# Kernel tuning notes

Hardware: AMD Instinct MI355X
Metric: run time of the kernel (lower is better)

Reference implementation:

```python
import jax, jax.numpy as jnp
import numpy as np

D_MODEL = 768
N_HEADS = 12
HEAD_DIM = D_MODEL // N_HEADS


def setup_inputs() -> dict:
    key = jax.random.key(0)
    ks = jax.random.split(key, 9)
    s = 1.0 / np.sqrt(D_MODEL)
    inp = {
        "inputs": jax.random.normal(ks[0], (1, 4096, D_MODEL), dtype=jnp.float32),
        "Wq": jax.random.uniform(ks[1], (D_MODEL, D_MODEL), jnp.float32, -s, s),
        "bq": jax.random.uniform(ks[2], (D_MODEL,), jnp.float32, -s, s),
        "Wk": jax.random.uniform(ks[3], (D_MODEL, D_MODEL), jnp.float32, -s, s),
        "bk": jax.random.uniform(ks[4], (D_MODEL,), jnp.float32, -s, s),
        "Wv": jax.random.uniform(ks[5], (D_MODEL, D_MODEL), jnp.float32, -s, s),
        "bv": jax.random.uniform(ks[6], (D_MODEL,), jnp.float32, -s, s),
        "Wo": jax.random.uniform(ks[7], (D_MODEL, D_MODEL), jnp.float32, -s, s),
        "bo": jax.random.uniform(ks[8], (D_MODEL,), jnp.float32, -s, s),
    }
    return inp


def reference(inputs, Wq, bq, Wk, bk, Wv, bv, Wo, bo):
    B, S, D = inputs.shape
    H, Hd = N_HEADS, HEAD_DIM

    def split_heads(x):  # [B,S,D] -> [B,H,S,Hd]
        return x.reshape(B, S, H, Hd).transpose(0, 2, 1, 3)

    # nn.Linear computes x @ W.T + b
    Q = split_heads(inputs @ Wq.T + bq)
    K = split_heads(inputs @ Wk.T + bk)
    V = split_heads(inputs @ Wv.T + bv)

    scores = jnp.einsum("bhsd,bhtd->bhst", Q, K) / jnp.sqrt(jnp.float32(Hd))
    causal = jnp.tril(jnp.ones((S, S), dtype=bool))  # True = keep
    scores = jnp.where(causal, scores, -jnp.inf)
    attn = jax.nn.softmax(scores, axis=-1)  # dropout is identity in eval

    out = jnp.einsum("bhst,bhtd->bhsd", attn, V)
    out = out.transpose(0, 2, 1, 3).reshape(B, S, D)
    return out @ Wo.T + bo
```

## Files before the change

### kernel.cpp

```cpp
#include <hip/hip_runtime.h>
#include <stdint.h>

#define SEQ 4096
#define DM 768
#define NH 12
#define HD 64

typedef unsigned short u16;
typedef short short8 __attribute__((ext_vector_type(8)));
typedef float floatx4 __attribute__((ext_vector_type(4)));
typedef float floatx16 __attribute__((ext_vector_type(16)));

__device__ inline u16 f2b(float f) {
  union { float f; uint32_t u; } v; v.f = f;
  uint32_t u = v.u;
  return (u16)((u + 0x7fffu + ((u >> 16) & 1u)) >> 16);
}

__device__ inline float b2f(u16 x) {
  union { uint32_t u; float f; } v; v.u = ((uint32_t)x) << 16;
  return v.f;
}

#if defined(__has_builtin)
#if __has_builtin(__builtin_amdgcn_cvt_pk_bf16_f32)
#define HAVE_PK_BF16 1
#endif
#endif

__device__ inline uint32_t pk_bf16(float a, float b) {
#ifdef HAVE_PK_BF16
  typedef __bf16 bf16x2_t __attribute__((ext_vector_type(2)));
  union { bf16x2_t v; uint32_t u; } c;
  c.v = __builtin_amdgcn_cvt_pk_bf16_f32(a, b);
  return c.u;
#else
  uint32_t r;
  asm("v_cvt_pk_bf16_f32 %0, %1, %2" : "=v"(r) : "v"(a), "v"(b));
  return r;
#endif
}

__device__ inline void pl32swap(uint32_t& a, uint32_t& b) {
  asm("v_permlane32_swap_b32 %0, %1" : "+v"(a), "+v"(b));
}

__device__ inline void load_lds16(const void* g, void* l) {
  __builtin_amdgcn_global_load_lds(
      (const __attribute__((address_space(1))) uint32_t*)g,
      (__attribute__((address_space(3))) uint32_t*)l, 16, 0, 0);
}

__global__ __launch_bounds__(256) void convert_all(
    const float* __restrict__ X, const float* __restrict__ Wq,
    const float* __restrict__ Wk, const float* __restrict__ Wv,
    const float* __restrict__ Wo,
    u16* __restrict__ Xb, u16* __restrict__ Wqb, u16* __restrict__ Wkb,
    u16* __restrict__ Wvb, u16* __restrict__ Wob) {
  int t = blockIdx.x * 256 + threadIdx.x;
  const int NX = SEQ * DM / 4;
  const int NW = DM * DM / 4;
  const float* src; u16* dst; int off;
  if (t < NX)               { src = X;  dst = Xb;  off = t; }
  else if (t < NX + NW)     { src = Wq; dst = Wqb; off = t - NX; }
  else if (t < NX + 2 * NW) { src = Wk; dst = Wkb; off = t - NX - NW; }
  else if (t < NX + 3 * NW) { src = Wv; dst = Wvb; off = t - NX - 2 * NW; }
  else if (t < NX + 4 * NW) { src = Wo; dst = Wob; off = t - NX - 3 * NW; }
  else return;
  float4 v = *(const float4*)(src + (size_t)off * 4);
  uint2 o;
  o.x = pk_bf16(v.x, v.y);
  o.y = pk_bf16(v.z, v.w);
  *(uint2*)(dst + (size_t)off * 4) = o;
}

__global__ __launch_bounds__(256) void gemm_qkv(
    const u16* __restrict__ Xb,
    const u16* __restrict__ Wqb, const u16* __restrict__ Wkb,
    const u16* __restrict__ Wvb,
    const float* __restrict__ bq, const float* __restrict__ bk,
    const float* __restrict__ bv,
    u16* __restrict__ Qh, u16* __restrict__ Kh, u16* __restrict__ VtG) {
  const int p = blockIdx.x;
  const int wg = (p & 7) * 72 + (p >> 3);
  const int mb = wg / 18, nz = wg % 18;
  const int z = nz / 6;
  const int n0 = (nz % 6) * 128;
  const int m0 = mb * 128;

  const u16* W; const float* bias;
  if (z == 0)      { W = Wqb; bias = bq; }
  else if (z == 1) { W = Wkb; bias = bk; }
  else             { W = Wvb; bias = bv; }

  __shared__ u16 smem[32768];
  u16* As = smem;
  u16* Bs = smem + 16384;

  const int tid = threadIdx.x;
  const int wave = tid >> 6, lane = tid & 63;
  const int g = lane >> 4, ln = lane & 15;
  const int wm = (wave & 1) * 64, wn = (wave >> 1) * 64;
  const int srow = lane >> 3;
  const int schunk = (lane & 7) ^ srow;
  const int swz = ln & 7;

  floatx4 acc[4][4] = {};

  auto stage = [&](int k0, int buf) {
#pragma unroll
    for (int i = 0; i < 4; ++i) {
      int u = wave * 4 + i;
      load_lds16(Xb + (size_t)(m0 + u * 8 + srow) * DM + k0 + schunk * 8,
                 As + buf * 8192 + u * 512);
      load_lds16(W + (size_t)(n0 + u * 8 + srow) * DM + k0 + schunk * 8,
                 Bs + buf * 8192 + u * 512);
    }
  };

  stage(0, 0);

  for (int kt = 0; kt < 12; ++kt) {
    const int cur = kt & 1;
    __syncthreads();
    if (kt < 11) stage((kt + 1) * 64, cur ^ 1);
    const u16* Ac = As + cur * 8192;
    const u16* Bc = Bs + cur * 8192;
#pragma unroll
    for (int kh = 0; kh < 2; ++kh) {
      short8 af[4], bf[4];
#pragma unroll
      for (int mi = 0; mi < 4; ++mi)
        af[mi] = *(const short8*)(Ac + (wm + mi * 16 + ln) * 64 +
                                  ((kh * 4 + g) ^ swz) * 8);
#pragma unroll
      for (int ni = 0; ni < 4; ++ni)
        bf[ni] = *(const short8*)(Bc + (wn + ni * 16 + ln) * 64 +
                                  ((kh * 4 + g) ^ swz) * 8);
#pragma unroll
      for (int mi = 0; mi < 4; ++mi)
#pragma unroll
        for (int ni = 0; ni < 4; ++ni)
          acc[mi][ni] = __builtin_amdgcn_mfma_f32_16x16x32_bf16(
              af[mi], bf[ni], acc[mi][ni], 0, 0, 0);
    }
  }

  const float qscale = 0.125f * 1.44269504089f;
  const int hh0 = n0 >> 6;
  __syncthreads();
  u16* ep = smem;

  if (z == 2) {
#pragma unroll
    for (int mi = 0; mi < 4; ++mi) {
      int row0 = wm + mi * 16 + g * 4;
#pragma unroll
      for (int ni = 0; ni < 4; ++ni) {
        int col = wn + ni * 16 + ln;
        float b = bias[n0 + col];
        uint2 o;
        o.x = pk_bf16(acc[mi][ni][0] + b, acc[mi][ni][1] + b);
        o.y = pk_bf16(acc[mi][ni][2] + b, acc[mi][ni][3] + b);
        *(uint2*)(ep + col * 136 + row0) = o;
      }
    }
    __syncthreads();
#pragma unroll
    for (int t = 0; t < 8; ++t) {
      int unit = tid + t * 256;
      int dcol = unit >> 4, ch = unit & 15;
      int head = hh0 + (dcol >> 6), d = dcol & 63;
      short8 v = *(const short8*)(ep + dcol * 136 + ch * 8);
      *(short8*)(VtG + ((size_t)(head * 64 + d)) * SEQ + m0 + ch * 8) = v;
    }
  } else {
    u16* out = (z == 0) ? Qh : Kh;
    float cs = (z == 0) ? qscale : 1.0f;
#pragma unroll
    for (int mi = 0; mi < 4; ++mi) {
      int row0 = wm + mi * 16 + g * 4;
#pragma unroll
      for (int ni = 0; ni < 4; ++ni) {
        int col = wn + ni * 16 + ln;
        float b = bias[n0 + col];
        uint32_t w0 = pk_bf16((acc[mi][ni][0] + b) * cs, (acc[mi][ni][1] + b) * cs);
        uint32_t w1 = pk_bf16((acc[mi][ni][2] + b) * cs, (acc[mi][ni][3] + b) * cs);
        ep[(row0 + 0) * 136 + col] = (u16)w0;
        ep[(row0 + 1) * 136 + col] = (u16)(w0 >> 16);
        ep[(row0 + 2) * 136 + col] = (u16)w1;
        ep[(row0 + 3) * 136 + col] = (u16)(w1 >> 16);
      }
    }
    __syncthreads();
#pragma unroll
    for (int t = 0; t < 8; ++t) {
      int unit = tid + t * 256;
      int row = unit >> 4, ch = unit & 15;
      int head = hh0 + (ch >> 3), d0 = (ch & 7) * 8;
      short8 v = *(const short8*)(ep + row * 136 + ch * 8);
      *(short8*)(out + ((size_t)head * SEQ + m0 + row) * HD + d0) = v;
    }
  }
}

#define CHUNK 16
#define M0 40.0f
__global__ __launch_bounds__(256, 4) void attn_chunk(
    const u16* __restrict__ Qh, const u16* __restrict__ Kh,
    const u16* __restrict__ VtG, u16* __restrict__ Opart,
    float* __restrict__ Lp) {
  const int p = blockIdx.y * NH + blockIdx.x;
  const int slot = p % 24, cyc = p / 24;
  const int qq = 3 * (slot & 7) + (slot >> 3);
  const int h = qq >> 1;
  const int b = 79 - (cyc * 2 + (qq & 1));
  int qB, ci;
  if (b < 8)       { qB = b;               ci = 0; }
  else if (b < 24) { int r = b - 8;  qB = 8 + (r >> 1); ci = r & 1; }
  else if (b < 48) { int r = b - 24; int d = r / 3; qB = 16 + d; ci = r - d * 3; }
  else             { int r = b - 48; qB = 24 + (r >> 2); ci = r & 3; }
  const int kb0 = ci * CHUNK;
  const int kb1 = min(kb0 + CHUNK, 2 * qB + 2);
  const int slot2 = (h * 32 + qB) * 4 + ci;

  const int tid = threadIdx.x, wave = tid >> 6, lane = tid & 63;
  const int hi = lane >> 5, lq = lane & 31;
  const int q0 = qB * 128;
  const int qwave = q0 + wave * 32;
  const int srow = lane >> 3;
  const int schunk = (lane & 7) ^ srow;
  const int rsw = lane & 7;

  __shared__ u16 Ks[2 * 4096];
  __shared__ u16 Vt[2 * 4096];

  const int qglob = qwave + lq;
  const u16* Qbase = Qh + ((size_t)h * SEQ + qglob) * HD;
  short8 aq[4];
#pragma unroll
  for (int s = 0; s < 4; ++s)
    aq[s] = *(const short8*)(Qbase + s * 16 + hi * 8);

  floatx16 oacc[2] = {};
  floatx4 lacc = {};

  const size_t kbase = (size_t)h * SEQ * HD;
  const size_t vbase = (size_t)h * 64 * SEQ;

  auto stage = [&](int kbIdx, int buf) {
#pragma unroll
    for (int i = 0; i < 2; ++i) {
      int u = wave * 2 + i;
      load_lds16(Kh + kbase + (size_t)(kbIdx * 64 + u * 8 + srow) * HD + schunk * 8,
                 Ks + buf * 4096 + u * 512);
      load_lds16(VtG + vbase + (size_t)(u * 8 + srow) * SEQ + kbIdx * 64 + schunk * 8,
                 Vt + buf * 4096 + u * 512);
    }
  };

  stage(kb0, 0);

  for (int kb = kb0; kb < kb1; ++kb) {
    const int cur = (kb - kb0) & 1;
    __syncthreads();
    if (kb + 1 < kb1) stage(kb + 1, cur ^ 1);

    const u16* Kc = Ks + cur * 4096;
    const u16* Vc = Vt + cur * 4096;

    if (kb * 64 > qwave + 31) continue;

    floatx16 st[2];
#pragma unroll
    for (int kblk = 0; kblk < 2; ++kblk)
#pragma unroll
      for (int r2 = 0; r2 < 16; ++r2) st[kblk][r2] = -M0;
    __builtin_amdgcn_s_setprio(1);
#pragma unroll
    for (int s = 0; s < 4; ++s)
#pragma unroll
      for (int kblk = 0; kblk < 2; ++kblk) {
        short8 kf = *(const short8*)(Kc + (kblk * 32 + lq) * 64 +
                                     ((s * 2 + hi) ^ rsw) * 8);
        st[kblk] = __builtin_amdgcn_mfma_f32_32x32x16_bf16(kf, aq[s], st[kblk],
                                                           0, 0, 0);
      }
    __builtin_amdgcn_s_setprio(0);

    if (kb * 64 + 63 > qwave) {
#pragma unroll
      for (int kblk = 0; kblk < 2; ++kblk)
#pragma unroll
        for (int r2 = 0; r2 < 16; ++r2) {
          int key = kb * 64 + kblk * 32 + (r2 & 3) + 8 * (r2 >> 2) + 4 * hi;
          if (key > qglob) st[kblk][r2] = -1e30f;
        }
    }

    uint32_t w[2][8];
#pragma unroll
    for (int kblk = 0; kblk < 2; ++kblk) {
#pragma unroll
      for (int r2 = 0; r2 < 16; ++r2)
        st[kblk][r2] = __builtin_amdgcn_exp2f(st[kblk][r2]);
#pragma unroll
      for (int r2 = 0; r2 < 4; ++r2)
        lacc[r2] += st[kblk][r2] + st[kblk][4 + r2] + st[kblk][8 + r2] +
                    st[kblk][12 + r2];
#pragma unroll
      for (int i = 0; i < 8; ++i)
        w[kblk][i] = pk_bf16(st[kblk][2 * i], st[kblk][2 * i + 1]);
    }

    __builtin_amdgcn_s_setprio(1);
#pragma unroll
    for (int ks = 0; ks < 4; ++ks) {
      const int kblk = ks >> 1, base = (ks & 1) * 4;
      uint32_t d0 = w[kblk][base + 0], d2 = w[kblk][base + 2];
      uint32_t d1 = w[kblk][base + 1], d3 = w[kblk][base + 3];
      pl32swap(d0, d2);
      pl32swap(d1, d3);
      union { uint32_t u[4]; short8 s; } bp;
      bp.u[0] = d0; bp.u[1] = d1; bp.u[2] = d2; bp.u[3] = d3;
#pragma unroll
      for (int dblk = 0; dblk < 2; ++dblk) {
        short8 vf = *(const short8*)(Vc + (dblk * 32 + lq) * 64 +
                                     ((ks * 2 + hi) ^ rsw) * 8);
        oacc[dblk] = __builtin_amdgcn_mfma_f32_32x32x16_bf16(vf, bp.s, oacc[dblk],
                                                             0, 0, 0);
      }
    }
    __builtin_amdgcn_s_setprio(0);
  }

  float l_i = lacc[0] + lacc[1] + lacc[2] + lacc[3];
  l_i += __shfl_xor(l_i, 32);

  float inv = 1.f / l_i;
  int qloc = wave * 32 + lq;
  u16* Op = Opart + (size_t)slot2 * 8192 + qloc * 64;
#pragma unroll
  for (int dblk = 0; dblk < 2; ++dblk)
#pragma unroll
    for (int qd = 0; qd < 4; ++qd) {
      uint2 o;
      o.x = pk_bf16(oacc[dblk][qd * 4 + 0] * inv, oacc[dblk][qd * 4 + 1] * inv);
      o.y = pk_bf16(oacc[dblk][qd * 4 + 2] * inv, oacc[dblk][qd * 4 + 3] * inv);
      *(uint2*)(Op + dblk * 32 + qd * 8 + hi * 4) = o;
    }
  if (hi == 0) Lp[(size_t)slot2 * 128 + qloc] = l_i;
}

__global__ __launch_bounds__(256) void attn_merge(
    const u16* __restrict__ Opart, const float* __restrict__ Lp,
    u16* __restrict__ Ob) {
  const int h = blockIdx.x, qB = blockIdx.y;
  const int n = (qB >> 3) + 1;
  const int base = (h * 32 + qB) * 4;
  const int q = threadIdx.x >> 1;
  const int d0 = (threadIdx.x & 1) * 32;

  float L = 0.f;
  for (int i = 0; i < n; ++i) L += Lp[(size_t)(base + i) * 128 + q];
  float invL = 1.f / L;

  float acc[32];
#pragma unroll
  for (int jj = 0; jj < 32; ++jj) acc[jj] = 0.f;
  for (int i = 0; i < n; ++i) {
    float wi = Lp[(size_t)(base + i) * 128 + q] * invL;
    const u16* src = Opart + (size_t)(base + i) * 8192 + q * 64 + d0;
#pragma unroll
    for (int c = 0; c < 4; ++c) {
      short8 a = ((const short8*)src)[c];
#pragma unroll
      for (int jj = 0; jj < 8; ++jj) acc[c * 8 + jj] += wi * b2f((u16)a[jj]);
    }
  }

  u16* dst = Ob + (size_t)(qB * 128 + q) * DM + h * HD + d0;
#pragma unroll
  for (int c = 0; c < 4; ++c) {
    uint4 o;
    o.x = pk_bf16(acc[c * 8 + 0], acc[c * 8 + 1]);
    o.y = pk_bf16(acc[c * 8 + 2], acc[c * 8 + 3]);
    o.z = pk_bf16(acc[c * 8 + 4], acc[c * 8 + 5]);
    o.w = pk_bf16(acc[c * 8 + 6], acc[c * 8 + 7]);
    ((uint4*)dst)[c] = o;
  }
}

__global__ __launch_bounds__(256) void gemm_out(
    const u16* __restrict__ Ab, const u16* __restrict__ Wob,
    const float* __restrict__ bo, float* __restrict__ Cout) {
  __shared__ u16 smem[16384];

  const int tid = threadIdx.x;
  const int wave = tid >> 6, lane = tid & 63;
  const int g = lane >> 4, ln = lane & 15;
  const int m0 = blockIdx.y * 64, n0 = blockIdx.x * 64;
  const int wm = (wave & 1) * 32, wn = (wave >> 1) * 32;
  const int srow = lane >> 3;
  const int schunk = (lane & 7) ^ srow;
  const int swz = ln & 7;

  floatx4 acc[2][2] = {};

#pragma unroll
  for (int i = 0; i < 2; ++i) {
    int u = wave * 2 + i;
    load_lds16(Ab + (size_t)(m0 + u * 8 + srow) * DM + schunk * 8, smem + u * 512);
    load_lds16(Wob + (size_t)(n0 + u * 8 + srow) * DM + schunk * 8,
               smem + 8192 + u * 512);
  }

  for (int kt = 0; kt < 12; ++kt) {
    const int cur = kt & 1;
    __syncthreads();
    if (kt < 11) {
      const int k0 = (kt + 1) * 64, nb = cur ^ 1;
#pragma unroll
      for (int i = 0; i < 2; ++i) {
        int u = wave * 2 + i;
        load_lds16(Ab + (size_t)(m0 + u * 8 + srow) * DM + k0 + schunk * 8,
                   smem + nb * 4096 + u * 512);
        load_lds16(Wob + (size_t)(n0 + u * 8 + srow) * DM + k0 + schunk * 8,
                   smem + 8192 + nb * 4096 + u * 512);
      }
    }
    const u16* Ac = smem + cur * 4096;
    const u16* Bc = smem + 8192 + cur * 4096;
    short8 af[2][2], bf[2][2];
#pragma unroll
    for (int mi = 0; mi < 2; ++mi)
#pragma unroll
      for (int kh = 0; kh < 2; ++kh)
        af[mi][kh] = *(const short8*)(Ac + (wm + mi * 16 + ln) * 64 +
                                      ((kh * 4 + g) ^ swz) * 8);
#pragma unroll
    for (int ni = 0; ni < 2; ++ni)
#pragma unroll
      for (int kh = 0; kh < 2; ++kh)
        bf[ni][kh] = *(const short8*)(Bc + (wn + ni * 16 + ln) * 64 +
                                      ((kh * 4 + g) ^ swz) * 8);
#pragma unroll
    for (int kh = 0; kh < 2; ++kh)
#pragma unroll
      for (int mi = 0; mi < 2; ++mi)
#pragma unroll
        for (int ni = 0; ni < 2; ++ni)
          acc[mi][ni] = __builtin_amdgcn_mfma_f32_16x16x32_bf16(
              af[mi][kh], bf[ni][kh], acc[mi][ni], 0, 0, 0);
  }

#pragma unroll
  for (int mi = 0; mi < 2; ++mi) {
    int row = m0 + wm + mi * 16 + g * 4;
#pragma unroll
    for (int ni = 0; ni < 2; ++ni) {
      int col = n0 + wn + ni * 16 + ln;
      float b = bo[col];
#pragma unroll
      for (int r = 0; r < 4; ++r)
        Cout[(size_t)(row + r) * DM + col] = acc[mi][ni][r] + b;
    }
  }
}

extern "C" void kernel_launch(void* const* d_in, const int* in_sizes, int n_in,
                              void* d_out, int out_size, void* d_ws, size_t ws_size,
                              hipStream_t stream) {
  const float* X  = (const float*)d_in[0];
  const float* Wq = (const float*)d_in[1];
  const float* bq = (const float*)d_in[2];
  const float* Wk = (const float*)d_in[3];
  const float* bk = (const float*)d_in[4];
  const float* Wv = (const float*)d_in[5];
  const float* bv = (const float*)d_in[6];
  const float* Wo = (const float*)d_in[7];
  const float* bo = (const float*)d_in[8];
  float* out = (float*)d_out;

  char* ws = (char*)d_ws;
  u16* Wob = (u16*)ws; ws += (size_t)DM * DM * 2;
  u16* Qh  = (u16*)ws; ws += (size_t)NH * SEQ * HD * 2;
  u16* Kh  = (u16*)ws; ws += (size_t)NH * SEQ * HD * 2;
  u16* VtG = (u16*)ws; ws += (size_t)NH * SEQ * HD * 2;
  u16* Ob  = (u16*)ws; ws += (size_t)SEQ * DM * 2;
  float* Lp = (float*)ws; ws += (size_t)NH * 32 * 4 * 128 * 4;
  char* ovl = ws;
  u16* Xb  = (u16*)ovl;
  u16* Wqb = Xb + (size_t)SEQ * DM;
  u16* Wkb = Wqb + (size_t)DM * DM;
  u16* Wvb = Wkb + (size_t)DM * DM;
  u16* Opart = (u16*)ovl;

  convert_all<<<5376, 256, 0, stream>>>(X, Wq, Wk, Wv, Wo, Xb, Wqb, Wkb, Wvb, Wob);

  gemm_qkv<<<576, 256, 0, stream>>>(Xb, Wqb, Wkb, Wvb, bq, bk, bv, Qh, Kh, VtG);

  dim3 ga(NH, 80);
  attn_chunk<<<ga, 256, 0, stream>>>(Qh, Kh, VtG, Opart, Lp);

  dim3 gm(NH, 32);
  attn_merge<<<gm, 256, 0, stream>>>(Opart, Lp, Ob);

  dim3 go(DM / 64, SEQ / 64);
  gemm_out<<<go, 256, 0, stream>>>(Ob, Wob, bo, out);
}
```

Measured before the change: 166.2 us.

## Fuse split-K attention merge into chunk kernel via last-arriver atomic counter

Removes the separate attn_merge launch. Each attention chunk block increments a per-(head, query-block) counter, and the last block to arrive combines the partial outputs with the L weights and writes Ob directly. Query blocks with a single chunk skip the partial buffers and write Ob straight away. The counters are zeroed inside convert_all. This saves a kernel launch and the partial round trip for small query blocks, at the cost of threadfences, an atomic, and a serial merge tail in the last-arriving block.

Result: slower. 236.0 us (+42.0%).

```diff
diff --git a/kernel.cpp b/kernel.cpp
--- a/kernel.cpp
+++ b/kernel.cpp
@@ -56,7 +56,10 @@
     const float* __restrict__ Wk, const float* __restrict__ Wv,
     const float* __restrict__ Wo,
     u16* __restrict__ Xb, u16* __restrict__ Wqb, u16* __restrict__ Wkb,
-    u16* __restrict__ Wvb, u16* __restrict__ Wob) {
+    u16* __restrict__ Wvb, u16* __restrict__ Wob, uint32_t* __restrict__ Cnt) {
+  if (blockIdx.x == 0) {
+    for (int i = threadIdx.x; i < NH * 32; i += 256) Cnt[i] = 0;
+  }
   int t = blockIdx.x * 256 + threadIdx.x;
   const int NX = SEQ * DM / 4;
   const int NW = DM * DM / 4;
@@ -209,7 +212,8 @@
 __global__ __launch_bounds__(256, 4) void attn_chunk(
     const u16* __restrict__ Qh, const u16* __restrict__ Kh,
     const u16* __restrict__ VtG, u16* __restrict__ Opart,
-    float* __restrict__ Lp) {
+    float* __restrict__ Lp, uint32_t* __restrict__ Cnt,
+    u16* __restrict__ Ob) {
   const int p = blockIdx.y * NH + blockIdx.x;
   const int slot = p % 24, cyc = p / 24;
   const int qq = 3 * (slot & 7) + (slot >> 3);
@@ -222,6 +226,7 @@
   else             { int r = b - 48; qB = 24 + (r >> 2); ci = r & 3; }
   const int kb0 = ci * CHUNK;
   const int kb1 = min(kb0 + CHUNK, 2 * qB + 2);
+  const int n_part = (qB >> 3) + 1;
   const int slot2 = (h * 32 + qB) * 4 + ci;
 
   const int tid = threadIdx.x, wave = tid >> 6, lane = tid & 63;
@@ -234,6 +239,7 @@
 
   __shared__ u16 Ks[2 * 4096];
   __shared__ u16 Vt[2 * 4096];
+  __shared__ int who;
 
   const int qglob = qwave + lq;
   const u16* Qbase = Qh + ((size_t)h * SEQ + qglob) * HD;
@@ -339,6 +345,21 @@
 
   float inv = 1.f / l_i;
   int qloc = wave * 32 + lq;
+
+  if (n_part == 1) {
+    u16* dst = Ob + (size_t)(q0 + qloc) * DM + h * HD;
+#pragma unroll
+    for (int dblk = 0; dblk < 2; ++dblk)
+#pragma unroll
+      for (int qd = 0; qd < 4; ++qd) {
+        uint2 o;
+        o.x = pk_bf16(oacc[dblk][qd * 4 + 0] * inv, oacc[dblk][qd * 4 + 1] * inv);
+        o.y = pk_bf16(oacc[dblk][qd * 4 + 2] * inv, oacc[dblk][qd * 4 + 3] * inv);
+        *(uint2*)(dst + dblk * 32 + qd * 8 + hi * 4) = o;
+      }
+    return;
+  }
+
   u16* Op = Opart + (size_t)slot2 * 8192 + qloc * 64;
 #pragma unroll
   for (int dblk = 0; dblk < 2; ++dblk)
@@ -350,44 +371,50 @@
       *(uint2*)(Op + dblk * 32 + qd * 8 + hi * 4) = o;
     }
   if (hi == 0) Lp[(size_t)slot2 * 128 + qloc] = l_i;
-}
-
-__global__ __launch_bounds__(256) void attn_merge(
-    const u16* __restrict__ Opart, const float* __restrict__ Lp,
-    u16* __restrict__ Ob) {
-  const int h = blockIdx.x, qB = blockIdx.y;
-  const int n = (qB >> 3) + 1;
-  const int base = (h * 32 + qB) * 4;
-  const int q = threadIdx.x >> 1;
-  const int d0 = (threadIdx.x & 1) * 32;
-
-  float L = 0.f;
-  for (int i = 0; i < n; ++i) L += Lp[(size_t)(base + i) * 128 + q];
-  float invL = 1.f / L;
-
-  float acc[32];
-#pragma unroll
-  for (int jj = 0; jj < 32; ++jj) acc[jj] = 0.f;
-  for (int i = 0; i < n; ++i) {
-    float wi = Lp[(size_t)(base + i) * 128 + q] * invL;
-    const u16* src = Opart + (size_t)(base + i) * 8192 + q * 64 + d0;
+
+  __syncthreads();
+  if (tid == 0) {
+    __threadfence();
+    uint32_t old = atomicAdd(&Cnt[h * 32 + qB], 1u);
+    who = (old == (uint32_t)(n_part - 1)) ? 1 : 0;
+  }
+  __syncthreads();
+  if (!who) return;
+  __threadfence();
+
+  {
+    const int base = (h * 32 + qB) * 4;
+    const int q = tid >> 1;
+    const int d0 = (tid & 1) * 32;
+
+    float L = 0.f;
+    for (int i = 0; i < n_part; ++i) L += Lp[(size_t)(base + i) * 128 + q];
+    float invL = 1.f / L;
+
+    float acc2[32];
+#pragma unroll
+    for (int jj = 0; jj < 32; ++jj) acc2[jj] = 0.f;
+    for (int i = 0; i < n_part; ++i) {
+      float wi = Lp[(size_t)(base + i) * 128 + q] * invL;
+      const u16* src = Opart + (size_t)(base + i) * 8192 + q * 64 + d0;
+#pragma unroll
+      for (int c = 0; c < 4; ++c) {
+        short8 a = ((const short8*)src)[c];
+#pragma unroll
+        for (int jj = 0; jj < 8; ++jj) acc2[c * 8 + jj] += wi * b2f((u16)a[jj]);
+      }
+    }
+
+    u16* dst = Ob + (size_t)(q0 + q) * DM + h * HD + d0;
 #pragma unroll
     for (int c = 0; c < 4; ++c) {
-      short8 a = ((const short8*)src)[c];
-#pragma unroll
-      for (int jj = 0; jj < 8; ++jj) acc[c * 8 + jj] += wi * b2f((u16)a[jj]);
-    }
-  }
-
-  u16* dst = Ob + (size_t)(qB * 128 + q) * DM + h * HD + d0;
-#pragma unroll
-  for (int c = 0; c < 4; ++c) {
-    uint4 o;
-    o.x = pk_bf16(acc[c * 8 + 0], acc[c * 8 + 1]);
-    o.y = pk_bf16(acc[c * 8 + 2], acc[c * 8 + 3]);
-    o.z = pk_bf16(acc[c * 8 + 4], acc[c * 8 + 5]);
-    o.w = pk_bf16(acc[c * 8 + 6], acc[c * 8 + 7]);
-    ((uint4*)dst)[c] = o;
+      uint4 o;
+      o.x = pk_bf16(acc2[c * 8 + 0], acc2[c * 8 + 1]);
+      o.y = pk_bf16(acc2[c * 8 + 2], acc2[c * 8 + 3]);
+      o.z = pk_bf16(acc2[c * 8 + 4], acc2[c * 8 + 5]);
+      o.w = pk_bf16(acc2[c * 8 + 6], acc2[c * 8 + 7]);
+      ((uint4*)dst)[c] = o;
+    }
   }
 }
 
@@ -489,6 +516,7 @@
   u16* VtG = (u16*)ws; ws += (size_t)NH * SEQ * HD * 2;
   u16* Ob  = (u16*)ws; ws += (size_t)SEQ * DM * 2;
   float* Lp = (float*)ws; ws += (size_t)NH * 32 * 4 * 128 * 4;
+  uint32_t* Cnt = (uint32_t*)ws; ws += (size_t)NH * 32 * 4;
   char* ovl = ws;
   u16* Xb  = (u16*)ovl;
   u16* Wqb = Xb + (size_t)SEQ * DM;
@@ -496,15 +524,13 @@
   u16* Wvb = Wkb + (size_t)DM * DM;
   u16* Opart = (u16*)ovl;
 
-  convert_all<<<5376, 256, 0, stream>>>(X, Wq, Wk, Wv, Wo, Xb, Wqb, Wkb, Wvb, Wob);
+  convert_all<<<5376, 256, 0, stream>>>(X, Wq, Wk, Wv, Wo, Xb, Wqb, Wkb, Wvb,
+                                        Wob, Cnt);
 
   gemm_qkv<<<576, 256, 0, stream>>>(Xb, Wqb, Wkb, Wvb, bq, bk, bv, Qh, Kh, VtG);
 
   dim3 ga(NH, 80);
-  attn_chunk<<<ga, 256, 0, stream>>>(Qh, Kh, VtG, Opart, Lp);
-
-  dim3 gm(NH, 32);
-  attn_merge<<<gm, 256, 0, stream>>>(Opart, Lp, Ob);
+  attn_chunk<<<ga, 256, 0, stream>>>(Qh, Kh, VtG, Opart, Lp, Cnt, Ob);
 
   dim3 go(DM / 64, SEQ / 64);
   gemm_out<<<go, 256, 0, stream>>>(Ob, Wob, bo, out);
```

## Fuse split-KV attention merge into output projection GEMM A-tile loading

Applied to the files above, without the earlier changes.

Removes the separate attn_merge kernel and the Ob intermediate buffer. The attention kernel now writes unnormalized partial outputs. The output GEMM sums up to four partials per row as it loads each A tile, scales them by the inverse total denominator and writes the bf16 result into LDS, overlapped with the MFMA work on the other buffer. This saves a kernel launch and a global write/read round trip of the merged activations. In exchange, every column block of the GEMM redoes the merge, so partial reads are multiplied, and the A loads become register-staged instead of direct-to-LDS.

New measurement: 191.7 us. 1.15x slower.

```diff
diff --git a/kernel.cpp b/kernel.cpp
--- a/kernel.cpp
+++ b/kernel.cpp
@@ -337,7 +337,6 @@
   float l_i = lacc[0] + lacc[1] + lacc[2] + lacc[3];
   l_i += __shfl_xor(l_i, 32);
 
-  float inv = 1.f / l_i;
   int qloc = wave * 32 + lq;
   u16* Op = Opart + (size_t)slot2 * 8192 + qloc * 64;
 #pragma unroll
@@ -345,54 +344,16 @@
 #pragma unroll
     for (int qd = 0; qd < 4; ++qd) {
       uint2 o;
-      o.x = pk_bf16(oacc[dblk][qd * 4 + 0] * inv, oacc[dblk][qd * 4 + 1] * inv);
-      o.y = pk_bf16(oacc[dblk][qd * 4 + 2] * inv, oacc[dblk][qd * 4 + 3] * inv);
+      o.x = pk_bf16(oacc[dblk][qd * 4 + 0], oacc[dblk][qd * 4 + 1]);
+      o.y = pk_bf16(oacc[dblk][qd * 4 + 2], oacc[dblk][qd * 4 + 3]);
       *(uint2*)(Op + dblk * 32 + qd * 8 + hi * 4) = o;
     }
   if (hi == 0) Lp[(size_t)slot2 * 128 + qloc] = l_i;
 }
 
-__global__ __launch_bounds__(256) void attn_merge(
+__global__ __launch_bounds__(256) void gemm_out(
     const u16* __restrict__ Opart, const float* __restrict__ Lp,
-    u16* __restrict__ Ob) {
-  const int h = blockIdx.x, qB = blockIdx.y;
-  const int n = (qB >> 3) + 1;
-  const int base = (h * 32 + qB) * 4;
-  const int q = threadIdx.x >> 1;
-  const int d0 = (threadIdx.x & 1) * 32;
-
-  float L = 0.f;
-  for (int i = 0; i < n; ++i) L += Lp[(size_t)(base + i) * 128 + q];
-  float invL = 1.f / L;
-
-  float acc[32];
-#pragma unroll
-  for (int jj = 0; jj < 32; ++jj) acc[jj] = 0.f;
-  for (int i = 0; i < n; ++i) {
-    float wi = Lp[(size_t)(base + i) * 128 + q] * invL;
-    const u16* src = Opart + (size_t)(base + i) * 8192 + q * 64 + d0;
-#pragma unroll
-    for (int c = 0; c < 4; ++c) {
-      short8 a = ((const short8*)src)[c];
-#pragma unroll
-      for (int jj = 0; jj < 8; ++jj) acc[c * 8 + jj] += wi * b2f((u16)a[jj]);
-    }
-  }
-
-  u16* dst = Ob + (size_t)(qB * 128 + q) * DM + h * HD + d0;
-#pragma unroll
-  for (int c = 0; c < 4; ++c) {
-    uint4 o;
-    o.x = pk_bf16(acc[c * 8 + 0], acc[c * 8 + 1]);
-    o.y = pk_bf16(acc[c * 8 + 2], acc[c * 8 + 3]);
-    o.z = pk_bf16(acc[c * 8 + 4], acc[c * 8 + 5]);
-    o.w = pk_bf16(acc[c * 8 + 6], acc[c * 8 + 7]);
-    ((uint4*)dst)[c] = o;
-  }
-}
-
-__global__ __launch_bounds__(256) void gemm_out(
-    const u16* __restrict__ Ab, const u16* __restrict__ Wob,
+    const u16* __restrict__ Wob,
     const float* __restrict__ bo, float* __restrict__ Cout) {
   __shared__ u16 smem[16384];
 
@@ -405,29 +366,71 @@
   const int schunk = (lane & 7) ^ srow;
   const int swz = ln & 7;
 
+  const int qB = m0 >> 7;
+  const int np = (qB >> 3) + 1;
+  const int ql0 = (m0 + (wave * 2 + 0) * 8 + srow) & 127;
+  const int ql1 = (m0 + (wave * 2 + 1) * 8 + srow) & 127;
+
   floatx4 acc[2][2] = {};
 
-#pragma unroll
-  for (int i = 0; i < 2; ++i) {
-    int u = wave * 2 + i;
-    load_lds16(Ab + (size_t)(m0 + u * 8 + srow) * DM + schunk * 8, smem + u * 512);
-    load_lds16(Wob + (size_t)(n0 + u * 8 + srow) * DM + schunk * 8,
-               smem + 8192 + u * 512);
+  auto loadA = [&](int kt, short8 pa[2][4], float lw[2]) {
+    const size_t sb = (size_t)(kt * 32 + qB) * 4;
+#pragma unroll
+    for (int uu = 0; uu < 2; ++uu) {
+      const int qloc = uu ? ql1 : ql0;
+      float L = 0.f;
+#pragma unroll
+      for (int i = 0; i < 4; ++i)
+        if (i < np) {
+          pa[uu][i] = *(const short8*)(Opart + (sb + i) * 8192 +
+                                       (size_t)qloc * 64 + schunk * 8);
+          L += Lp[(sb + i) * 128 + qloc];
+        }
+      lw[uu] = 1.f / L;
+    }
+  };
+  auto writeA = [&](const short8 pa[2][4], const float lw[2], int buf) {
+#pragma unroll
+    for (int uu = 0; uu < 2; ++uu) {
+      const int u = wave * 2 + uu;
+      float a[8];
+#pragma unroll
+      for (int j = 0; j < 8; ++j) a[j] = b2f((u16)pa[uu][0][j]);
+#pragma unroll
+      for (int i = 1; i < 4; ++i)
+        if (i < np)
+#pragma unroll
+          for (int j = 0; j < 8; ++j) a[j] += b2f((u16)pa[uu][i][j]);
+      union { uint32_t u32[4]; short8 s; } o;
+#pragma unroll
+      for (int j = 0; j < 4; ++j)
+        o.u32[j] = pk_bf16(a[2 * j] * lw[uu], a[2 * j + 1] * lw[uu]);
+      *(short8*)(smem + buf * 4096 + u * 512 + lane * 8) = o.s;
+    }
+  };
+  auto stageB = [&](int k0, int buf) {
+#pragma unroll
+    for (int i = 0; i < 2; ++i) {
+      int u = wave * 2 + i;
+      load_lds16(Wob + (size_t)(n0 + u * 8 + srow) * DM + k0 + schunk * 8,
+                 smem + 8192 + buf * 4096 + u * 512);
+    }
+  };
+
+  {
+    short8 pa[2][4]; float lw[2];
+    stageB(0, 0);
+    loadA(0, pa, lw);
+    writeA(pa, lw, 0);
   }
 
   for (int kt = 0; kt < 12; ++kt) {
     const int cur = kt & 1;
     __syncthreads();
+    short8 pa[2][4]; float lw[2];
     if (kt < 11) {
-      const int k0 = (kt + 1) * 64, nb = cur ^ 1;
-#pragma unroll
-      for (int i = 0; i < 2; ++i) {
-        int u = wave * 2 + i;
-        load_lds16(Ab + (size_t)(m0 + u * 8 + srow) * DM + k0 + schunk * 8,
-                   smem + nb * 4096 + u * 512);
-        load_lds16(Wob + (size_t)(n0 + u * 8 + srow) * DM + k0 + schunk * 8,
-                   smem + 8192 + nb * 4096 + u * 512);
-      }
+      stageB((kt + 1) * 64, cur ^ 1);
+      loadA(kt + 1, pa, lw);
     }
     const u16* Ac = smem + cur * 4096;
     const u16* Bc = smem + 8192 + cur * 4096;
@@ -452,6 +455,7 @@
         for (int ni = 0; ni < 2; ++ni)
           acc[mi][ni] = __builtin_amdgcn_mfma_f32_16x16x32_bf16(
               af[mi][kh], bf[ni][kh], acc[mi][ni], 0, 0, 0);
+    if (kt < 11) writeA(pa, lw, cur ^ 1);
   }
 
 #pragma unroll
@@ -487,7 +491,6 @@
   u16* Qh  = (u16*)ws; ws += (size_t)NH * SEQ * HD * 2;
   u16* Kh  = (u16*)ws; ws += (size_t)NH * SEQ * HD * 2;
   u16* VtG = (u16*)ws; ws += (size_t)NH * SEQ * HD * 2;
-  u16* Ob  = (u16*)ws; ws += (size_t)SEQ * DM * 2;
   float* Lp = (float*)ws; ws += (size_t)NH * 32 * 4 * 128 * 4;
   char* ovl = ws;
   u16* Xb  = (u16*)ovl;
@@ -496,16 +499,14 @@
   u16* Wvb = Wkb + (size_t)DM * DM;
   u16* Opart = (u16*)ovl;
 
-  convert_all<<<5376, 256, 0, stream>>>(X, Wq, Wk, Wv, Wo, Xb, Wqb, Wkb, Wvb, Wob);
+  convert_all<<<5376, 256, 0, stream>>>(X, Wq, Wk, Wv, Wo, Xb, Wqb, Wkb, Wvb,
+                                        Wob);
 
   gemm_qkv<<<576, 256, 0, stream>>>(Xb, Wqb, Wkb, Wvb, bq, bk, bv, Qh, Kh, VtG);
 
   dim3 ga(NH, 80);
   attn_chunk<<<ga, 256, 0, stream>>>(Qh, Kh, VtG, Opart, Lp);
 
-  dim3 gm(NH, 32);
-  attn_merge<<<gm, 256, 0, stream>>>(Opart, Lp, Ob);
-
   dim3 go(DM / 64, SEQ / 64);
-  gemm_out<<<go, 256, 0, stream>>>(Ob, Wob, bo, out);
-}
+  gemm_out<<<go, 256, 0, stream>>>(Opart, Lp, Wob, bo, out);
+}
```
